# Optimization experiments

Measured on AMD Instinct MI355X. Metric: run time of the kernel, lower is better.

The kernel has to match this reference:

```python
import jax, jax.numpy as jnp
import numpy as np
import math

NCLASSES = 3
NMS_THR = 0.25
SCORE_THR = 0.1
MAX_NUM = 500
B, N = 4, 8192


def setup_inputs() -> dict:
    key = jax.random.key(0)
    ks = jax.random.split(key, 6)
    xy = jax.random.uniform(ks[0], (B, N, 2), minval=0.0, maxval=70.0)
    z = jax.random.normal(ks[1], (B, N, 1))
    lwh = jax.random.uniform(ks[2], (B, N, 3), minval=1.0, maxval=5.0)
    theta = jax.random.uniform(ks[3], (B, N, 1), minval=-math.pi, maxval=math.pi)
    cls = jax.random.uniform(ks[4], (B, N, NCLASSES))
    dirc = jax.random.randint(ks[5], (B, N, 1), 0, 2).astype(jnp.float32)
    results = jnp.concatenate([xy, z, lwh, theta, cls, dirc], axis=-1)  # [B,N,11]
    return {"results": results}


def limit_period(val, offset=1.0, period=math.pi):
    return val - jnp.floor(val / period + offset) * period


def _pairwise_iou(b):
    # b: [N,4] = (x1,y1,x2,y2); axis-aligned BEV IoU
    x1, y1, x2, y2 = b[:, 0], b[:, 1], b[:, 2], b[:, 3]
    area = (x2 - x1) * (y2 - y1)  # [N]
    iw = jnp.clip(jnp.minimum(x2[:, None], x2[None, :]) - jnp.maximum(x1[:, None], x1[None, :]), 0.0)
    ih = jnp.clip(jnp.minimum(y2[:, None], y2[None, :]) - jnp.maximum(y1[:, None], y1[None, :]), 0.0)
    inter = iw * ih
    return inter / (area[:, None] + area[None, :] - inter + 1e-8)


def _nms_class(boxes4, scores):
    # greedy NMS on score-descending order; invalid (below-threshold) boxes get -inf score
    valid = scores > SCORE_THR
    s = jnp.where(valid, scores, -jnp.inf)
    order = jnp.argsort(-s)  # descending
    bs = boxes4[order]
    ss = s[order]
    iou = _pairwise_iou(bs)  # [N,N]
    idx = jnp.arange(boxes4.shape[0])
    keep0 = jnp.isfinite(ss)

    def body(i, keep):
        sup = keep[i] & (iou[i] > NMS_THR) & (idx > i)
        return keep & ~sup

    keep = jax.lax.fori_loop(0, boxes4.shape[0], body, keep0)
    return order, jnp.where(keep, ss, -jnp.inf)


def _process(sample):
    # sample: [N,11] -> padded (bboxes [MAX_NUM,7], labels [MAX_NUM], scores [MAX_NUM])
    bbox = sample[:, :7]
    cls = sample[:, 7:10]
    dirp = sample[:, 10]
    xy = bbox[:, :2]
    lw = bbox[:, 3:5]
    boxes4 = jnp.concatenate([xy - lw / 2, xy + lw / 2], axis=-1)  # [N,4]

    all_b, all_l, all_s = [], [], []
    for c in range(NCLASSES):
        order, ss = _nms_class(boxes4, cls[:, c])
        bb = bbox[order]
        dd = dirp[order]
        ang = limit_period(bb[:, 6]) + (1.0 - dd) * math.pi
        bb = jnp.concatenate([bb[:, :6], ang[:, None]], axis=-1)
        all_b.append(bb)
        all_s.append(ss)
        all_l.append(jnp.full((N,), c, dtype=jnp.int32))
    b = jnp.concatenate(all_b, 0)   # [3N,7]
    s = jnp.concatenate(all_s, 0)   # [3N]
    l = jnp.concatenate(all_l, 0)   # [3N]
    top_s, top_i = jax.lax.top_k(s, MAX_NUM)
    return b[top_i], l[top_i], top_s


def reference(results):
    # results: [B,N,11]; returns (lidar_bboxes [B,500,7], labels [B,500], scores [B,500])
    return jax.vmap(_process)(results)
```

## Files before the change

### kernel.cpp

```cpp
#include <hip/hip_runtime.h>
#include <stdint.h>

#pragma clang fp contract(off)

#define NB 4
#define NN 8192
#define NC 3
#define NG 12
#define MAXN 500
#define KEEP_CAP 512

typedef unsigned long long u64;
typedef uint32_t u32;

#define NSO   0u
#define NSKEY 393216u
#define NSB4  786432u
#define NSAR  2359296u
#define NVAL  2752512u
#define NALV  2764800u
#define NKKEY 2777088u
#define NKPOS 2801664u
#define NKCNT 2826240u
#define NFLG  2826304u
#define PMAT  3145728u
#define WS_NEED 9437184u

#define PR_CH   32
#define PR_ROWS 2048
#define PUNITS_PER_G 528
#define PB_TPB 256
#define PB_BLOCKS 1584

#define WS_SORTED_ORIG 0
#define WS_ALIVE       393216
#define WS_KEPT_KEY    405504
#define WS_KEPT_POS    430080
#define WS_KEPT_CNT    454656
#define NMS_EPS 1.0000004f

__device__ __forceinline__ u32 sort_key(float s) {
  u32 b = __float_as_uint(s);
  u32 o = (b & 0x80000000u) ? ~b : (b | 0x80000000u);
  return ~o;
}

#define PHYS(i) ((i) + ((i) >> 3))
#define CEX(A, B, UP) \
  { if ((x[A] > x[B]) == (UP)) { u64 tt = x[A]; x[A] = x[B]; x[B] = tt; } }

__global__ __launch_bounds__(256) void sortL_kernel(
    const float* __restrict__ in, u64* __restrict__ kk)
{
  const int g = blockIdx.x >> 2, seg = blockIdx.x & 3;
  const int b = g / NC, c = g % NC;
  const float* __restrict__ base = in + (size_t)b * NN * 11;
  __shared__ u64 sk[2304];
  const int tid = threadIdx.x;
  const int gbase = seg << 11;

  for (int i = tid; i < 2048; i += 256) {
    int p = gbase + i;
    float sc = base[p * 11 + 7 + c];
    float s = (sc > 0.1f) ? sc : -INFINITY;
    sk[PHYS(i)] = ((u64)sort_key(s) << 16) | (u32)p;
  }
  __syncthreads();
  {
    const int pb = 9 * tid;
    u64 x[8];
#pragma unroll
    for (int a = 0; a < 8; ++a) x[a] = sk[pb + a];
    const bool u8 = ((((tid << 3)) & 8) == 0);
    CEX(0, 1, true); CEX(2, 3, false); CEX(4, 5, true); CEX(6, 7, false);
    CEX(0, 2, true); CEX(1, 3, true); CEX(4, 6, false); CEX(5, 7, false);
    CEX(0, 1, true); CEX(2, 3, true); CEX(4, 5, false); CEX(6, 7, false);
    CEX(0, 4, u8); CEX(1, 5, u8); CEX(2, 6, u8); CEX(3, 7, u8);
    CEX(0, 2, u8); CEX(1, 3, u8); CEX(4, 6, u8); CEX(5, 7, u8);
    CEX(0, 1, u8); CEX(2, 3, u8); CEX(4, 5, u8); CEX(6, 7, u8);
#pragma unroll
    for (int a = 0; a < 8; ++a) sk[pb + a] = x[a];
  }
  __syncthreads();
  for (int k = 16; k <= 2048; k <<= 1) {
    for (int j = k >> 1; j >= 8; j >>= 1) {
      for (int t = tid; t < 1024; t += 256) {
        int i = (t << 1) - (t & (j - 1));
        int q = i | j;
        int pi = PHYS(i), pq = PHYS(q);
        u64 ka = sk[pi], kb = sk[pq];
        bool up = ((i & k) == 0);
        if ((ka > kb) == up) { sk[pi] = kb; sk[pq] = ka; }
      }
      __syncthreads();
    }
    {
      const int lb = tid << 3;
      const bool up = ((lb & k) == 0);
      const int pb = 9 * tid;
      u64 x[8];
#pragma unroll
      for (int a = 0; a < 8; ++a) x[a] = sk[pb + a];
      CEX(0, 4, up); CEX(1, 5, up); CEX(2, 6, up); CEX(3, 7, up);
      CEX(0, 2, up); CEX(1, 3, up); CEX(4, 6, up); CEX(5, 7, up);
      CEX(0, 1, up); CEX(2, 3, up); CEX(4, 5, up); CEX(6, 7, up);
#pragma unroll
      for (int a = 0; a < 8; ++a) sk[pb + a] = x[a];
    }
    __syncthreads();
  }
  for (int i = tid; i < 2048; i += 256)
    kk[(size_t)g * NN + gbase + i] = sk[PHYS(i)];
}

__global__ __launch_bounds__(1024) void merge_kernel(
    const float* __restrict__ in, const u64* __restrict__ kk,
    u32* __restrict__ so, u32* __restrict__ skey, float4* __restrict__ sb4,
    float* __restrict__ sar, u64* __restrict__ valid)
{
  const int g = blockIdx.x;
  const int b = g / NC;
  const int tid = threadIdx.x;
  __shared__ u64 seg[NN];
  __shared__ u64 outk[PR_ROWS];
  const u64* __restrict__ ks = kk + (size_t)g * NN;

  for (int e = tid; e < NN; e += 1024) seg[e] = ks[e];
  __syncthreads();

  for (int e = tid; e < NN; e += 1024) {
    const int sg = e >> 11, idx = e & 2047;
    const u64 k = seg[e];
    int rank = idx;
#pragma unroll
    for (int os = 0; os < 4; ++os) {
      if (os == sg) continue;
      const u64* __restrict__ arr = seg + (os << 11);
      int pos = 0;
#pragma unroll
      for (int st = 1024; st > 0; st >>= 1) {
        int np = pos + st;
        if (np <= 2048 && arr[np - 1] < k) pos = np;
      }
      rank += pos;
    }
    if (rank < PR_ROWS) outk[rank] = k;
  }
  __syncthreads();

  const float* __restrict__ base = in + (size_t)b * NN * 11;
  const int lane = tid & 63;
#pragma unroll
  for (int it = 0; it < PR_ROWS / 1024; ++it) {
    int i = it * 1024 + tid;
    u64 kv = outk[i];
    int orig = (int)(kv & 0xFFFFu);
    u32 key32 = (u32)(kv >> 16);
    so[(size_t)g * NN + i] = (u32)orig;
    skey[(size_t)g * NN + i] = key32;
    const float* r = base + orig * 11;
    float x = r[0], y = r[1], l = r[3], wd = r[4];
    float hx = l * 0.5f, hy = wd * 0.5f;
    float x1 = x - hx, y1 = y - hy, x2 = x + hx, y2 = y + hy;
    sb4[(size_t)g * NN + i] = make_float4(x1, y1, x2, y2);
    sar[(size_t)g * NN + i] = (x2 - x1) * (y2 - y1);
    u64 bal = __ballot(key32 != 0xFF800000u);
    if (lane == 0) valid[g * 128 + (i >> 6)] = bal;
  }
}

__global__ __launch_bounds__(PB_TPB) void build_prefix_kernel(
    const float4* __restrict__ sb4, const float* __restrict__ sar,
    u64* __restrict__ pmat)
{
  const int wib = __builtin_amdgcn_readfirstlane((int)(threadIdx.x >> 6));
  const int lane = threadIdx.x & 63;
  const int W = blockIdx.x * (PB_TPB / 64) + wib;
  if (W >= NG * PUNITS_PER_G) return;
  const int g = W / PUNITS_PER_G;
  int r = W - g * PUNITS_PER_G;
  int rb = 0, cum = 0;
  while (r >= cum + (PR_CH - rb)) { cum += PR_CH - rb; ++rb; }
  const int jw = rb + (r - cum);
  const double CMULT = 0.25 * (1.0 + 0x1p-24);

  const int col = jw * 64 + lane;
  const float4 J = sb4[(size_t)g * NN + col];
  const float jar = sar[(size_t)g * NN + col];
  const float4* __restrict__ Ib = sb4 + (size_t)g * NN + rb * 64;
  const float* __restrict__ Ia = sar + (size_t)g * NN + rb * 64;

  u32 accLo = 0, accHi = 0;
  for (int rr = 0; rr < 64; ++rr) {
    const float4 I = Ib[rr];
    const float iar = Ia[rr];
    const bool sel = (lane == rr);
    float iw = fminf(I.z, J.z) - fmaxf(I.x, J.x);
    float ih = fminf(I.w, J.w) - fmaxf(I.y, J.y);
    iw = fmaxf(iw, 0.0f); ih = fmaxf(ih, 0.0f);
    float inter = iw * ih;
    float denom = ((iar + jar) - inter) + 1e-8f;
    u64 cand = __ballot((double)inter > CMULT * (double)denom);
    accLo = sel ? (u32)(cand & 0xffffffffu) : accLo;
    accHi = sel ? (u32)(cand >> 32) : accHi;
  }
  pmat[((size_t)(g * PR_CH + jw)) * PR_ROWS + rb * 64 + lane] =
      ((u64)accHi << 32) | accLo;
}

__global__ __launch_bounds__(1024) void scan_prefix_kernel(
    const u64* __restrict__ pmat, const u64* __restrict__ valid,
    const u32* __restrict__ skey, u32* __restrict__ kept_key,
    u32* __restrict__ kept_pos, u32* __restrict__ kept_cnt,
    u32* __restrict__ flags)
{
  const int g = blockIdx.x;
  const int tid = threadIdx.x;
  const int wv = tid >> 6, lane = tid & 63;
  const int wl = tid & 127, grp = tid >> 7;
  __shared__ u64 remv[PR_CH];
  __shared__ u64 keepw[PR_CH];
  __shared__ u64 keepS;
  __shared__ u32 prefixL[PR_CH];
  __shared__ u32 cntS;
  __shared__ int stopS;

  if (tid < PR_CH) { remv[tid] = ~valid[g * 128 + tid]; keepw[tid] = 0; }
  if (tid == 0) { cntS = 0; stopS = 0; }
  __syncthreads();

  const u64* __restrict__ pm = pmat + (size_t)g * PR_CH * PR_ROWS;
  u64 rwDiag = 0, rwDiagNext = 0;
  if (wv == 0) rwDiag = pm[lane];
  const u64 maskgt = (lane == 63) ? 0ull : (~0ull << (lane + 1));

  for (int cc = 0; cc < PR_CH; ++cc) {
    const int w = cc + 1 + wl;
    const bool act = (w < PR_CH);
    u64 rw[8];
    if (act) {
#pragma unroll
      for (int k = 0; k < 8; ++k)
        rw[k] = pm[(size_t)w * PR_ROWS + cc * 64 + grp * 8 + k];
    }
    if (wv == 0) {
      const u64 alive0 = ~remv[cc];
      u64 K = alive0;
      for (int it = 0; it < 64; ++it) {
        u64 contrib = ((K >> lane) & 1ull) ? (rwDiag & maskgt) : 0ull;
#pragma unroll
        for (int off = 32; off > 0; off >>= 1)
          contrib |= (u64)__shfl_xor((long long)contrib, off);
        u64 Knew = alive0 & ~contrib;
        if (Knew == K) break;
        K = Knew;
      }
      if (lane == 0) {
        keepw[cc] = K; keepS = K;
        cntS += (u32)__popcll(K);
        if (cntS >= KEEP_CAP) stopS = 1;
      }
      if (cc + 1 < PR_CH)
        rwDiagNext = pm[(size_t)(cc + 1) * PR_ROWS + (cc + 1) * 64 + lane];
    }
    __syncthreads();
    if (stopS) break;
    if (act) {
      const u32 kmg = (u32)((keepS >> (grp * 8)) & 0xffu);
      u64 acc = 0;
#pragma unroll
      for (int k = 0; k < 8; ++k)
        if ((kmg >> k) & 1u) acc |= rw[k];
      if (acc) atomicOr(&remv[w], acc);
    }
    if (wv == 0) rwDiag = rwDiagNext;
    __syncthreads();
  }
  __syncthreads();

  if (tid == 0) {
    u32 acc = 0;
    for (int i = 0; i < PR_CH; ++i) { prefixL[i] = acc; acc += (u32)__popcll(keepw[i]); }
    cntS = acc;
    u32 ok = (acc >= KEEP_CAP) ? 1u : 0u;
    flags[g] = ok;
    if (ok) kept_cnt[g] = KEEP_CAP;
  }
  __syncthreads();
  if (cntS < KEEP_CAP) return;
  for (int p = tid; p < PR_ROWS; p += 1024) {
    int wd = p >> 6;
    u64 kw = keepw[wd];
    if ((kw >> (p & 63)) & 1ull) {
      u32 rank = prefixL[wd] + (u32)__popcll(kw & ((1ull << (p & 63)) - 1ull));
      if (rank < KEEP_CAP) {
        kept_key[g * KEEP_CAP + rank] = skey[g * NN + p];
        kept_pos[g * KEEP_CAP + rank] = (u32)p;
      }
    }
  }
}

__global__ __launch_bounds__(1024) void nms_kernel(
    const float* __restrict__ in, u32* __restrict__ sorted_orig,
    u64* __restrict__ alive_out, u32* __restrict__ kept_key,
    u32* __restrict__ kept_pos, u32* __restrict__ kept_cnt,
    const u32* __restrict__ flags)
{
  const int g = blockIdx.x;
  if (flags != nullptr && flags[g]) return;
  const int b = g / NC, c = g % NC;
  const float* __restrict__ base = in + (size_t)b * NN * 11;
  __shared__ u32 keys[NN];
  __shared__ uint16_t sidx[NN];
  __shared__ float4 keeperBuf[2][64];
  __shared__ int nkBuf[2];
  __shared__ u64 aliveArr[128];
  __shared__ u32 prefix[128];
  const int tid = threadIdx.x;
  const int w = tid >> 6, lane = tid & 63;

  for (int p = tid; p < NN; p += 1024) {
    float sc = base[p * 11 + 7 + c];
    float s = (sc > 0.1f) ? sc : -INFINITY;
    keys[p] = sort_key(s);
    sidx[p] = (uint16_t)p;
  }
  __syncthreads();
  for (int k = 2; k <= NN; k <<= 1) {
    for (int j = k >> 1; j > 0; j >>= 1) {
      for (int t = tid; t < NN / 2; t += 1024) {
        int i = (t << 1) - (t & (j - 1));
        int q = i | j;
        u32 ka = keys[i], kb = keys[q];
        uint16_t ia = sidx[i], ib = sidx[q];
        bool gt = (ka > kb) || (ka == kb && ia > ib);
        bool up = ((i & k) == 0);
        if (gt == up) { keys[i] = kb; keys[q] = ka; sidx[i] = ib; sidx[q] = ia; }
      }
      __syncthreads();
    }
  }
  float bx1[8], by1[8], bx2[8], by2[8], barea[8];
  u64 alive[8];
#pragma unroll
  for (int k = 0; k < 8; ++k) {
    int p = k * 1024 + tid;
    u32 key = keys[p];
    int orig = sidx[p];
    sorted_orig[g * NN + p] = (u32)orig;
    const float* r = base + orig * 11;
    float x = r[0], y = r[1], l = r[3], wd = r[4];
    float hx = l * 0.5f, hy = wd * 0.5f;
    bx1[k] = x - hx; by1[k] = y - hy; bx2[k] = x + hx; by2[k] = y + hy;
    barea[k] = (bx2[k] - bx1[k]) * (by2[k] - by1[k]);
    alive[k] = __ballot(key != 0xFF800000u);
  }
  for (int cc = 0; cc < 128; ++cc) {
    __syncthreads();
    int nk_prev = (cc > 0) ? nkBuf[(cc - 1) & 1] : 0;
    if (nk_prev > 0) {
      const int par = (cc - 1) & 1;
      for (int j = 0; j < nk_prev; ++j) {
        float4 K = keeperBuf[par][j];
        float ka = (K.z - K.x) * (K.w - K.y);
#pragma unroll
        for (int k = 0; k < 8; ++k) {
          if ((k * 16 + w) < cc) continue;
          if (alive[k] == 0ull) continue;
          float iw = fminf(bx2[k], K.z) - fmaxf(bx1[k], K.x);
          float ih = fminf(by2[k], K.w) - fmaxf(by1[k], K.y);
          iw = fmaxf(iw, 0.0f); ih = fmaxf(ih, 0.0f);
          float inter = iw * ih;
          float denom = (barea[k] + ka) - inter + 1e-8f;
          float t = 0.25f * denom;
          u64 sup = __ballot(inter > t);
          u64 wnd = __ballot(inter > t && inter <= t * NMS_EPS);
          if (wnd) {
            bool bb = inter > t;
            if (bb && inter <= t * NMS_EPS) bb = (inter / denom) > 0.25f;
            sup = __ballot(bb);
          }
          alive[k] &= ~sup;
        }
      }
    }
    if (w == (cc & 15)) {
      float mx1 = 0.f, my1 = 0.f, mx2 = 0.f, my2 = 0.f, ma = 0.f;
      u64 m = 0ull;
#pragma unroll
      for (int k = 0; k < 8; ++k) if (k == (cc >> 4)) {
        mx1 = bx1[k]; my1 = by1[k]; mx2 = bx2[k]; my2 = by2[k]; ma = barea[k];
        m = alive[k];
      }
      u64 keepm = 0ull;
      int nk = 0;
      while (m) {
        int bp = __ffsll(m) - 1;
        keepm |= 1ull << bp;
        m &= ~(1ull << bp);
        float kx1 = __shfl(mx1, bp), ky1 = __shfl(my1, bp);
        float kx2 = __shfl(mx2, bp), ky2 = __shfl(my2, bp);
        float ka = (kx2 - kx1) * (ky2 - ky1);
        float iw = fminf(mx2, kx2) - fmaxf(mx1, kx1);
        float ih = fminf(my2, ky2) - fmaxf(my1, ky1);
        iw = fmaxf(iw, 0.0f); ih = fmaxf(ih, 0.0f);
        float inter = iw * ih;
        float denom = (ma + ka) - inter + 1e-8f;
        float t = 0.25f * denom;
        u64 sup = __ballot(inter > t);
        u64 wnd = __ballot(inter > t && inter <= t * NMS_EPS);
        if (wnd) {
          bool bb = inter > t;
          if (bb && inter <= t * NMS_EPS) bb = (inter / denom) > 0.25f;
          sup = __ballot(bb);
        }
        m &= ~sup;
        if (lane == bp) keeperBuf[cc & 1][nk] = make_float4(mx1, my1, mx2, my2);
        nk++;
      }
#pragma unroll
      for (int k = 0; k < 8; ++k) if (k == (cc >> 4)) alive[k] = keepm;
      if (lane == 0) nkBuf[cc & 1] = nk;
    }
  }
  __syncthreads();
  if (lane == 0) {
#pragma unroll
    for (int k = 0; k < 8; ++k) aliveArr[k * 16 + w] = alive[k];
  }
  __syncthreads();
  if (tid == 0) {
    u32 acc = 0;
    for (int i = 0; i < 128; ++i) { prefix[i] = acc; acc += (u32)__popcll(aliveArr[i]); }
    kept_cnt[g] = acc;
  }
  __syncthreads();
  for (int i = tid; i < 128; i += 1024) alive_out[g * 128 + i] = aliveArr[i];
#pragma unroll
  for (int k = 0; k < 8; ++k) {
    int word = k * 16 + w;
    u64 a = alive[k];
    if ((a >> lane) & 1ull) {
      u32 rank = prefix[word] + (u32)__popcll(a & ((1ull << lane) - 1ull));
      if (rank < KEEP_CAP) {
        int p = k * 1024 + tid;
        kept_key[g * KEEP_CAP + rank] = keys[p];
        kept_pos[g * KEEP_CAP + rank] = (u32)p;
      }
    }
  }
}

__global__ __launch_bounds__(512) void topk_kernel(
    const float* __restrict__ in, const u32* __restrict__ sorted_orig,
    const u64* __restrict__ alive_ws, const u32* __restrict__ kept_key,
    const u32* __restrict__ kept_pos, const u32* __restrict__ kept_cnt,
    float* __restrict__ out)
{
  const int b = blockIdx.x;
  const int tid = threadIdx.x;
  __shared__ u64 arr[NC][KEEP_CAP];
  __shared__ int sT[3], sL[3];
  if (tid < 3) {
    int K = (int)kept_cnt[b * 3 + tid];
    sT[tid] = K;
    sL[tid] = min(K, KEEP_CAP);
  }
  __syncthreads();
  const int L0 = sL[0], L1 = sL[1], L2 = sL[2];
  const int navail = L0 + L1 + L2;
  const int Ttot = sT[0] + sT[1] + sT[2];

  for (int s = tid; s < NC * KEEP_CAP; s += 512) {
    int c = s >> 9, i = s & 511;
    u64 key = ~0ull;
    if (i < sL[c]) {
      int g = b * 3 + c;
      u64 k32 = kept_key[g * KEEP_CAP + i];
      u32 pos = kept_pos[g * KEEP_CAP + i];
      key = (k32 << 15) | (u32)(c * NN + pos);
    }
    arr[c][i] = key;
  }
  __syncthreads();

  for (int s = tid; s < NC * KEEP_CAP; s += 512) {
    int c = s >> 9, i = s & 511;
    if (i >= sL[c]) continue;
    u64 k = arr[c][i];
    int rank = i;
#pragma unroll
    for (int oc = 0; oc < NC; ++oc) {
      if (oc == c) continue;
      int lo = 0, hi = sL[oc];
      while (lo < hi) { int mid = (lo + hi) >> 1; if (arr[oc][mid] < k) lo = mid + 1; else hi = mid; }
      rank += lo;
    }
    if (rank < MAXN) {
      u32 flat = (u32)(k & 32767u);
      int cc = (int)(flat >> 13), pos = (int)(flat & 8191);
      u32 k32 = (u32)(k >> 15);
      u32 o = ~k32;
      u32 bits = (o & 0x80000000u) ? (o ^ 0x80000000u) : ~o;
      float sval = __uint_as_float(bits);
      u32 orig = sorted_orig[(b * 3 + cc) * NN + pos];
      const float* row = in + ((size_t)b * NN + orig) * 11;
      const float PI_F = 3.14159265358979323846f;
      float theta = row[6];
      float v = theta / PI_F;
      float fl = floorf(v + 1.0f);
      float lp = theta - fl * PI_F;
      float ang = lp + (1.0f - row[10]) * PI_F;
      float* ob = out + ((size_t)b * MAXN + rank) * 7;
      ob[0] = row[0]; ob[1] = row[1]; ob[2] = row[2];
      ob[3] = row[3]; ob[4] = row[4]; ob[5] = row[5]; ob[6] = ang;
      out[NB * MAXN * 7 + b * MAXN + rank] = (float)cc;
      out[NB * MAXN * 7 + NB * MAXN + b * MAXN + rank] = sval;
    }
  }

  for (int r = navail + tid; r < MAXN; r += 512) {
    int need = r - Ttot;
    int fflat = 0;
    for (int wd = 0; wd < 384; ++wd) {
      u64 a = alive_ws[b * 384 + wd];
      int z = 64 - __popcll(a);
      if (need < z) {
        u64 na = ~a;
        for (int it = 0; it < need; ++it) na &= na - 1ull;
        fflat = wd * 64 + (__ffsll(na) - 1);
        break;
      }
      need -= z;
    }
    int c = fflat >> 13, pos = fflat & 8191;
    u32 orig = sorted_orig[(b * 3 + c) * NN + pos];
    const float* row = in + ((size_t)b * NN + orig) * 11;
    const float PI_F = 3.14159265358979323846f;
    float theta = row[6];
    float v = theta / PI_F;
    float fl = floorf(v + 1.0f);
    float lp = theta - fl * PI_F;
    float ang = lp + (1.0f - row[10]) * PI_F;
    float* ob = out + ((size_t)b * MAXN + r) * 7;
    ob[0] = row[0]; ob[1] = row[1]; ob[2] = row[2];
    ob[3] = row[3]; ob[4] = row[4]; ob[5] = row[5]; ob[6] = ang;
    out[NB * MAXN * 7 + b * MAXN + r] = (float)c;
    out[NB * MAXN * 7 + NB * MAXN + b * MAXN + r] = -INFINITY;
  }
}

extern "C" void kernel_launch(void* const* d_in, const int* in_sizes, int n_in,
                              void* d_out, int out_size, void* d_ws, size_t ws_size,
                              hipStream_t stream) {
  const float* in = (const float*)d_in[0];
  float* out = (float*)d_out;
  char* ws = (char*)d_ws;

  if (ws_size >= (size_t)WS_NEED) {
    u32* so = (u32*)(ws + NSO);
    u32* skey = (u32*)(ws + NSKEY);
    float4* sb4 = (float4*)(ws + NSB4);
    float* sar = (float*)(ws + NSAR);
    u64* valid = (u64*)(ws + NVAL);
    u64* alive = (u64*)(ws + NALV);
    u32* kkey = (u32*)(ws + NKKEY);
    u32* kpos = (u32*)(ws + NKPOS);
    u32* kcnt = (u32*)(ws + NKCNT);
    u32* flags = (u32*)(ws + NFLG);
    u64* pmat = (u64*)(ws + PMAT);
    u64* kk = (u64*)(ws + PMAT);

    sortL_kernel<<<dim3(48), dim3(256), 0, stream>>>(in, kk);
    merge_kernel<<<dim3(NG), dim3(1024), 0, stream>>>(
        in, kk, so, skey, sb4, sar, valid);
    build_prefix_kernel<<<dim3(PB_BLOCKS), dim3(PB_TPB), 0, stream>>>(
        sb4, sar, pmat);
    scan_prefix_kernel<<<dim3(NG), dim3(1024), 0, stream>>>(
        pmat, valid, skey, kkey, kpos, kcnt, flags);
    nms_kernel<<<dim3(NG), dim3(1024), 0, stream>>>(
        in, so, alive, kkey, kpos, kcnt, flags);
    topk_kernel<<<dim3(NB), dim3(512), 0, stream>>>(
        in, so, alive, kkey, kpos, kcnt, out);
  } else {
    u32* sorted_orig = (u32*)(ws + WS_SORTED_ORIG);
    u64* alive = (u64*)(ws + WS_ALIVE);
    u32* kept_key = (u32*)(ws + WS_KEPT_KEY);
    u32* kept_pos = (u32*)(ws + WS_KEPT_POS);
    u32* kept_cnt = (u32*)(ws + WS_KEPT_CNT);
    nms_kernel<<<dim3(NG), dim3(1024), 0, stream>>>(
        in, sorted_orig, alive, kept_key, kept_pos, kept_cnt, nullptr);
    topk_kernel<<<dim3(NB), dim3(512), 0, stream>>>(
        in, sorted_orig, alive, kept_key, kept_pos, kept_cnt, out);
  }
}
```

Baseline: 100.1 us.

## Fuse six-kernel NMS pipeline into one cooperative kernel with grid syncs

Replaces the chain of separate launches (local sort, merge, IoU prefix build, prefix scan, fallback NMS, top-k) with a single 48-block, 1024-thread cooperative kernel that separates the stages with grid.sync(). The goal is to remove per-launch overhead and the gaps between kernels in a pipeline made of many short stages. In exchange, the IoU-matrix build now runs on only 48 blocks instead of 1584 smaller ones, and each grid barrier has a cost, so the parallel-heavy stage could slow down.

```diff
diff --git a/kernel.cpp b/kernel.cpp
--- a/kernel.cpp
+++ b/kernel.cpp
@@ -1,7 +1,10 @@
 #include <hip/hip_runtime.h>
+#include <hip/hip_cooperative_groups.h>
 #include <stdint.h>
 
 #pragma clang fp contract(off)
+
+namespace cg = cooperative_groups;
 
 #define NB 4
 #define NN 8192
@@ -12,6 +15,7 @@
 
 typedef unsigned long long u64;
 typedef uint32_t u32;
+typedef uint16_t u16;
 
 #define NSO   0u
 #define NSKEY 393216u
@@ -29,8 +33,6 @@
 #define PR_CH   32
 #define PR_ROWS 2048
 #define PUNITS_PER_G 528
-#define PB_TPB 256
-#define PB_BLOCKS 1584
 
 #define WS_SORTED_ORIG 0
 #define WS_ALIVE       393216
@@ -49,253 +51,497 @@
 #define CEX(A, B, UP) \
   { if ((x[A] > x[B]) == (UP)) { u64 tt = x[A]; x[A] = x[B]; x[B] = tt; } }
 
-__global__ __launch_bounds__(256) void sortL_kernel(
-    const float* __restrict__ in, u64* __restrict__ kk)
+__global__ __launch_bounds__(1024) void fused_kernel(
+    const float* __restrict__ in, u64* __restrict__ kk, u32* __restrict__ so,
+    u32* __restrict__ skey, float4* __restrict__ sb4, float* __restrict__ sar,
+    u64* __restrict__ valid, u64* __restrict__ pmat, u64* __restrict__ alive,
+    u32* __restrict__ kkey, u32* __restrict__ kpos, u32* __restrict__ kcnt,
+    u32* __restrict__ flags, float* __restrict__ out)
 {
-  const int g = blockIdx.x >> 2, seg = blockIdx.x & 3;
-  const int b = g / NC, c = g % NC;
-  const float* __restrict__ base = in + (size_t)b * NN * 11;
-  __shared__ u64 sk[2304];
+  cg::grid_group grid = cg::this_grid();
+  __shared__ __align__(16) unsigned char smemraw[81920];
   const int tid = threadIdx.x;
-  const int gbase = seg << 11;
-
-  for (int i = tid; i < 2048; i += 256) {
-    int p = gbase + i;
-    float sc = base[p * 11 + 7 + c];
-    float s = (sc > 0.1f) ? sc : -INFINITY;
-    sk[PHYS(i)] = ((u64)sort_key(s) << 16) | (u32)p;
-  }
-  __syncthreads();
+  const int blk = blockIdx.x;
+  const int lane = tid & 63;
+
   {
-    const int pb = 9 * tid;
-    u64 x[8];
-#pragma unroll
-    for (int a = 0; a < 8; ++a) x[a] = sk[pb + a];
-    const bool u8 = ((((tid << 3)) & 8) == 0);
-    CEX(0, 1, true); CEX(2, 3, false); CEX(4, 5, true); CEX(6, 7, false);
-    CEX(0, 2, true); CEX(1, 3, true); CEX(4, 6, false); CEX(5, 7, false);
-    CEX(0, 1, true); CEX(2, 3, true); CEX(4, 5, false); CEX(6, 7, false);
-    CEX(0, 4, u8); CEX(1, 5, u8); CEX(2, 6, u8); CEX(3, 7, u8);
-    CEX(0, 2, u8); CEX(1, 3, u8); CEX(4, 6, u8); CEX(5, 7, u8);
-    CEX(0, 1, u8); CEX(2, 3, u8); CEX(4, 5, u8); CEX(6, 7, u8);
-#pragma unroll
-    for (int a = 0; a < 8; ++a) sk[pb + a] = x[a];
-  }
-  __syncthreads();
-  for (int k = 16; k <= 2048; k <<= 1) {
-    for (int j = k >> 1; j >= 8; j >>= 1) {
-      for (int t = tid; t < 1024; t += 256) {
-        int i = (t << 1) - (t & (j - 1));
-        int q = i | j;
-        int pi = PHYS(i), pq = PHYS(q);
-        u64 ka = sk[pi], kb = sk[pq];
-        bool up = ((i & k) == 0);
-        if ((ka > kb) == up) { sk[pi] = kb; sk[pq] = ka; }
-      }
-      __syncthreads();
-    }
-    {
-      const int lb = tid << 3;
-      const bool up = ((lb & k) == 0);
+    u64* sk = (u64*)smemraw;
+    const int g = blk >> 2, seg = blk & 3;
+    const int b = g / NC, c = g % NC;
+    const float* __restrict__ base = in + (size_t)b * NN * 11;
+    const int gbase = seg << 11;
+
+    for (int i = tid; i < 2048; i += 1024) {
+      int p = gbase + i;
+      float sc = base[p * 11 + 7 + c];
+      float s = (sc > 0.1f) ? sc : -INFINITY;
+      sk[PHYS(i)] = ((u64)sort_key(s) << 16) | (u32)p;
+    }
+    __syncthreads();
+    if (tid < 256) {
       const int pb = 9 * tid;
       u64 x[8];
 #pragma unroll
       for (int a = 0; a < 8; ++a) x[a] = sk[pb + a];
-      CEX(0, 4, up); CEX(1, 5, up); CEX(2, 6, up); CEX(3, 7, up);
-      CEX(0, 2, up); CEX(1, 3, up); CEX(4, 6, up); CEX(5, 7, up);
-      CEX(0, 1, up); CEX(2, 3, up); CEX(4, 5, up); CEX(6, 7, up);
+      const bool u8 = ((((tid << 3)) & 8) == 0);
+      CEX(0, 1, true); CEX(2, 3, false); CEX(4, 5, true); CEX(6, 7, false);
+      CEX(0, 2, true); CEX(1, 3, true); CEX(4, 6, false); CEX(5, 7, false);
+      CEX(0, 1, true); CEX(2, 3, true); CEX(4, 5, false); CEX(6, 7, false);
+      CEX(0, 4, u8); CEX(1, 5, u8); CEX(2, 6, u8); CEX(3, 7, u8);
+      CEX(0, 2, u8); CEX(1, 3, u8); CEX(4, 6, u8); CEX(5, 7, u8);
+      CEX(0, 1, u8); CEX(2, 3, u8); CEX(4, 5, u8); CEX(6, 7, u8);
 #pragma unroll
       for (int a = 0; a < 8; ++a) sk[pb + a] = x[a];
     }
     __syncthreads();
-  }
-  for (int i = tid; i < 2048; i += 256)
-    kk[(size_t)g * NN + gbase + i] = sk[PHYS(i)];
-}
-
-__global__ __launch_bounds__(1024) void merge_kernel(
-    const float* __restrict__ in, const u64* __restrict__ kk,
-    u32* __restrict__ so, u32* __restrict__ skey, float4* __restrict__ sb4,
-    float* __restrict__ sar, u64* __restrict__ valid)
-{
-  const int g = blockIdx.x;
-  const int b = g / NC;
-  const int tid = threadIdx.x;
-  __shared__ u64 seg[NN];
-  __shared__ u64 outk[PR_ROWS];
-  const u64* __restrict__ ks = kk + (size_t)g * NN;
-
-  for (int e = tid; e < NN; e += 1024) seg[e] = ks[e];
-  __syncthreads();
-
-  for (int e = tid; e < NN; e += 1024) {
-    const int sg = e >> 11, idx = e & 2047;
-    const u64 k = seg[e];
-    int rank = idx;
-#pragma unroll
-    for (int os = 0; os < 4; ++os) {
-      if (os == sg) continue;
-      const u64* __restrict__ arr = seg + (os << 11);
-      int pos = 0;
-#pragma unroll
-      for (int st = 1024; st > 0; st >>= 1) {
-        int np = pos + st;
-        if (np <= 2048 && arr[np - 1] < k) pos = np;
-      }
-      rank += pos;
-    }
-    if (rank < PR_ROWS) outk[rank] = k;
-  }
-  __syncthreads();
-
-  const float* __restrict__ base = in + (size_t)b * NN * 11;
-  const int lane = tid & 63;
-#pragma unroll
-  for (int it = 0; it < PR_ROWS / 1024; ++it) {
-    int i = it * 1024 + tid;
-    u64 kv = outk[i];
-    int orig = (int)(kv & 0xFFFFu);
-    u32 key32 = (u32)(kv >> 16);
-    so[(size_t)g * NN + i] = (u32)orig;
-    skey[(size_t)g * NN + i] = key32;
-    const float* r = base + orig * 11;
-    float x = r[0], y = r[1], l = r[3], wd = r[4];
-    float hx = l * 0.5f, hy = wd * 0.5f;
-    float x1 = x - hx, y1 = y - hy, x2 = x + hx, y2 = y + hy;
-    sb4[(size_t)g * NN + i] = make_float4(x1, y1, x2, y2);
-    sar[(size_t)g * NN + i] = (x2 - x1) * (y2 - y1);
-    u64 bal = __ballot(key32 != 0xFF800000u);
-    if (lane == 0) valid[g * 128 + (i >> 6)] = bal;
-  }
-}
-
-__global__ __launch_bounds__(PB_TPB) void build_prefix_kernel(
-    const float4* __restrict__ sb4, const float* __restrict__ sar,
-    u64* __restrict__ pmat)
-{
-  const int wib = __builtin_amdgcn_readfirstlane((int)(threadIdx.x >> 6));
-  const int lane = threadIdx.x & 63;
-  const int W = blockIdx.x * (PB_TPB / 64) + wib;
-  if (W >= NG * PUNITS_PER_G) return;
-  const int g = W / PUNITS_PER_G;
-  int r = W - g * PUNITS_PER_G;
-  int rb = 0, cum = 0;
-  while (r >= cum + (PR_CH - rb)) { cum += PR_CH - rb; ++rb; }
-  const int jw = rb + (r - cum);
-  const double CMULT = 0.25 * (1.0 + 0x1p-24);
-
-  const int col = jw * 64 + lane;
-  const float4 J = sb4[(size_t)g * NN + col];
-  const float jar = sar[(size_t)g * NN + col];
-  const float4* __restrict__ Ib = sb4 + (size_t)g * NN + rb * 64;
-  const float* __restrict__ Ia = sar + (size_t)g * NN + rb * 64;
-
-  u32 accLo = 0, accHi = 0;
-  for (int rr = 0; rr < 64; ++rr) {
-    const float4 I = Ib[rr];
-    const float iar = Ia[rr];
-    const bool sel = (lane == rr);
-    float iw = fminf(I.z, J.z) - fmaxf(I.x, J.x);
-    float ih = fminf(I.w, J.w) - fmaxf(I.y, J.y);
-    iw = fmaxf(iw, 0.0f); ih = fmaxf(ih, 0.0f);
-    float inter = iw * ih;
-    float denom = ((iar + jar) - inter) + 1e-8f;
-    u64 cand = __ballot((double)inter > CMULT * (double)denom);
-    accLo = sel ? (u32)(cand & 0xffffffffu) : accLo;
-    accHi = sel ? (u32)(cand >> 32) : accHi;
-  }
-  pmat[((size_t)(g * PR_CH + jw)) * PR_ROWS + rb * 64 + lane] =
-      ((u64)accHi << 32) | accLo;
-}
-
-__global__ __launch_bounds__(1024) void scan_prefix_kernel(
-    const u64* __restrict__ pmat, const u64* __restrict__ valid,
-    const u32* __restrict__ skey, u32* __restrict__ kept_key,
-    u32* __restrict__ kept_pos, u32* __restrict__ kept_cnt,
-    u32* __restrict__ flags)
-{
-  const int g = blockIdx.x;
-  const int tid = threadIdx.x;
-  const int wv = tid >> 6, lane = tid & 63;
-  const int wl = tid & 127, grp = tid >> 7;
-  __shared__ u64 remv[PR_CH];
-  __shared__ u64 keepw[PR_CH];
-  __shared__ u64 keepS;
-  __shared__ u32 prefixL[PR_CH];
-  __shared__ u32 cntS;
-  __shared__ int stopS;
-
-  if (tid < PR_CH) { remv[tid] = ~valid[g * 128 + tid]; keepw[tid] = 0; }
-  if (tid == 0) { cntS = 0; stopS = 0; }
-  __syncthreads();
-
-  const u64* __restrict__ pm = pmat + (size_t)g * PR_CH * PR_ROWS;
-  u64 rwDiag = 0, rwDiagNext = 0;
-  if (wv == 0) rwDiag = pm[lane];
-  const u64 maskgt = (lane == 63) ? 0ull : (~0ull << (lane + 1));
-
-  for (int cc = 0; cc < PR_CH; ++cc) {
-    const int w = cc + 1 + wl;
-    const bool act = (w < PR_CH);
-    u64 rw[8];
-    if (act) {
-#pragma unroll
-      for (int k = 0; k < 8; ++k)
-        rw[k] = pm[(size_t)w * PR_ROWS + cc * 64 + grp * 8 + k];
-    }
-    if (wv == 0) {
-      const u64 alive0 = ~remv[cc];
-      u64 K = alive0;
-      for (int it = 0; it < 64; ++it) {
-        u64 contrib = ((K >> lane) & 1ull) ? (rwDiag & maskgt) : 0ull;
-#pragma unroll
-        for (int off = 32; off > 0; off >>= 1)
-          contrib |= (u64)__shfl_xor((long long)contrib, off);
-        u64 Knew = alive0 & ~contrib;
-        if (Knew == K) break;
-        K = Knew;
-      }
+    for (int k = 16; k <= 2048; k <<= 1) {
+      for (int j = k >> 1; j >= 8; j >>= 1) {
+        {
+          int t = tid;
+          int i = (t << 1) - (t & (j - 1));
+          int q = i | j;
+          int pi = PHYS(i), pq = PHYS(q);
+          u64 ka = sk[pi], kb = sk[pq];
+          bool up = ((i & k) == 0);
+          if ((ka > kb) == up) { sk[pi] = kb; sk[pq] = ka; }
+        }
+        __syncthreads();
+      }
+      if (tid < 256) {
+        const int lb = tid << 3;
+        const bool up = ((lb & k) == 0);
+        const int pb = 9 * tid;
+        u64 x[8];
+#pragma unroll
+        for (int a = 0; a < 8; ++a) x[a] = sk[pb + a];
+        CEX(0, 4, up); CEX(1, 5, up); CEX(2, 6, up); CEX(3, 7, up);
+        CEX(0, 2, up); CEX(1, 3, up); CEX(4, 6, up); CEX(5, 7, up);
+        CEX(0, 1, up); CEX(2, 3, up); CEX(4, 5, up); CEX(6, 7, up);
+#pragma unroll
+        for (int a = 0; a < 8; ++a) sk[pb + a] = x[a];
+      }
+      __syncthreads();
+    }
+    for (int i = tid; i < 2048; i += 1024)
+      kk[(size_t)g * NN + gbase + i] = sk[PHYS(i)];
+  }
+  grid.sync();
+
+  if (blk < NG) {
+    const int g = blk;
+    const int b = g / NC;
+    u64* seg = (u64*)smemraw;
+    u64* outk = (u64*)(smemraw + 65536);
+    const u64* __restrict__ ks = kk + (size_t)g * NN;
+
+    for (int e = tid; e < NN; e += 1024) seg[e] = ks[e];
+    __syncthreads();
+
+    for (int e = tid; e < NN; e += 1024) {
+      const int sg = e >> 11, idx = e & 2047;
+      const u64 k = seg[e];
+      int rank = idx;
+#pragma unroll
+      for (int os = 0; os < 4; ++os) {
+        if (os == sg) continue;
+        const u64* __restrict__ arr = seg + (os << 11);
+        int pos = 0;
+#pragma unroll
+        for (int st = 1024; st > 0; st >>= 1) {
+          int np = pos + st;
+          if (np <= 2048 && arr[np - 1] < k) pos = np;
+        }
+        rank += pos;
+      }
+      if (rank < PR_ROWS) outk[rank] = k;
+    }
+    __syncthreads();
+
+    const float* __restrict__ base = in + (size_t)b * NN * 11;
+#pragma unroll
+    for (int it = 0; it < PR_ROWS / 1024; ++it) {
+      int i = it * 1024 + tid;
+      u64 kv = outk[i];
+      int orig = (int)(kv & 0xFFFFu);
+      u32 key32 = (u32)(kv >> 16);
+      so[(size_t)g * NN + i] = (u32)orig;
+      skey[(size_t)g * NN + i] = key32;
+      const float* r = base + orig * 11;
+      float x = r[0], y = r[1], l = r[3], wd = r[4];
+      float hx = l * 0.5f, hy = wd * 0.5f;
+      float x1 = x - hx, y1 = y - hy, x2 = x + hx, y2 = y + hy;
+      sb4[(size_t)g * NN + i] = make_float4(x1, y1, x2, y2);
+      sar[(size_t)g * NN + i] = (x2 - x1) * (y2 - y1);
+      u64 bal = __ballot(key32 != 0xFF800000u);
+      if (lane == 0) valid[g * 128 + (i >> 6)] = bal;
+    }
+  }
+  grid.sync();
+
+  {
+    const int wib = __builtin_amdgcn_readfirstlane((int)(tid >> 6));
+    const double CMULT = 0.25 * (1.0 + 0x1p-24);
+    for (int W = blk * 16 + wib; W < NG * PUNITS_PER_G; W += 48 * 16) {
+      const int g = W / PUNITS_PER_G;
+      int r = W - g * PUNITS_PER_G;
+      int rb = 0, cum = 0;
+      while (r >= cum + (PR_CH - rb)) { cum += PR_CH - rb; ++rb; }
+      const int jw = rb + (r - cum);
+
+      const int col = jw * 64 + lane;
+      const float4 J = sb4[(size_t)g * NN + col];
+      const float jar = sar[(size_t)g * NN + col];
+      const float4* __restrict__ Ib = sb4 + (size_t)g * NN + rb * 64;
+      const float* __restrict__ Ia = sar + (size_t)g * NN + rb * 64;
+
+      u32 accLo = 0, accHi = 0;
+      for (int rr = 0; rr < 64; ++rr) {
+        const float4 I = Ib[rr];
+        const float iar = Ia[rr];
+        const bool sel = (lane == rr);
+        float iw = fminf(I.z, J.z) - fmaxf(I.x, J.x);
+        float ih = fminf(I.w, J.w) - fmaxf(I.y, J.y);
+        iw = fmaxf(iw, 0.0f); ih = fmaxf(ih, 0.0f);
+        float inter = iw * ih;
+        float denom = ((iar + jar) - inter) + 1e-8f;
+        u64 cand = __ballot((double)inter > CMULT * (double)denom);
+        accLo = sel ? (u32)(cand & 0xffffffffu) : accLo;
+        accHi = sel ? (u32)(cand >> 32) : accHi;
+      }
+      pmat[((size_t)(g * PR_CH + jw)) * PR_ROWS + rb * 64 + lane] =
+          ((u64)accHi << 32) | accLo;
+    }
+  }
+  grid.sync();
+
+  {
+    __shared__ u64 remv[PR_CH];
+    __shared__ u64 keepw[PR_CH];
+    __shared__ u64 keepS;
+    __shared__ u32 prefixL[PR_CH];
+    __shared__ u32 cntS;
+    __shared__ int stopS;
+    if (blk < NG) {
+      const int g = blk;
+      const int wv = tid >> 6;
+      const int wl = tid & 127, grp = tid >> 7;
+
+      if (tid < PR_CH) { remv[tid] = ~valid[g * 128 + tid]; keepw[tid] = 0; }
+      if (tid == 0) { cntS = 0; stopS = 0; }
+      __syncthreads();
+
+      const u64* __restrict__ pm = pmat + (size_t)g * PR_CH * PR_ROWS;
+      u64 rwDiag = 0, rwDiagNext = 0;
+      if (wv == 0) rwDiag = pm[lane];
+      const u64 maskgt = (lane == 63) ? 0ull : (~0ull << (lane + 1));
+
+      for (int cc = 0; cc < PR_CH; ++cc) {
+        const int w = cc + 1 + wl;
+        const bool act = (w < PR_CH);
+        u64 rw[8];
+        if (act) {
+#pragma unroll
+          for (int k = 0; k < 8; ++k)
+            rw[k] = pm[(size_t)w * PR_ROWS + cc * 64 + grp * 8 + k];
+        }
+        if (wv == 0) {
+          const u64 alive0 = ~remv[cc];
+          u64 K = alive0;
+          for (int it = 0; it < 64; ++it) {
+            u64 contrib = ((K >> lane) & 1ull) ? (rwDiag & maskgt) : 0ull;
+#pragma unroll
+            for (int off = 32; off > 0; off >>= 1)
+              contrib |= (u64)__shfl_xor((long long)contrib, off);
+            u64 Knew = alive0 & ~contrib;
+            if (Knew == K) break;
+            K = Knew;
+          }
+          if (lane == 0) {
+            keepw[cc] = K; keepS = K;
+            cntS += (u32)__popcll(K);
+            if (cntS >= KEEP_CAP) stopS = 1;
+          }
+          if (cc + 1 < PR_CH)
+            rwDiagNext = pm[(size_t)(cc + 1) * PR_ROWS + (cc + 1) * 64 + lane];
+        }
+        __syncthreads();
+        if (stopS) break;
+        if (act) {
+          const u32 kmg = (u32)((keepS >> (grp * 8)) & 0xffu);
+          u64 acc = 0;
+#pragma unroll
+          for (int k = 0; k < 8; ++k)
+            if ((kmg >> k) & 1u) acc |= rw[k];
+          if (acc) atomicOr(&remv[w], acc);
+        }
+        if (wv == 0) rwDiag = rwDiagNext;
+        __syncthreads();
+      }
+      __syncthreads();
+
+      if (tid == 0) {
+        u32 acc = 0;
+        for (int i = 0; i < PR_CH; ++i) { prefixL[i] = acc; acc += (u32)__popcll(keepw[i]); }
+        cntS = acc;
+        u32 ok = (acc >= KEEP_CAP) ? 1u : 0u;
+        flags[g] = ok;
+        if (ok) kcnt[g] = KEEP_CAP;
+      }
+      __syncthreads();
+      if (cntS >= KEEP_CAP) {
+        for (int p = tid; p < PR_ROWS; p += 1024) {
+          int wd = p >> 6;
+          u64 kw = keepw[wd];
+          if ((kw >> (p & 63)) & 1ull) {
+            u32 rank = prefixL[wd] + (u32)__popcll(kw & ((1ull << (p & 63)) - 1ull));
+            if (rank < KEEP_CAP) {
+              kkey[g * KEEP_CAP + rank] = skey[g * NN + p];
+              kpos[g * KEEP_CAP + rank] = (u32)p;
+            }
+          }
+        }
+      }
+    }
+  }
+  grid.sync();
+
+  {
+    __shared__ float4 keeperBuf[2][64];
+    __shared__ int nkBuf[2];
+    __shared__ u64 aliveArr[128];
+    __shared__ u32 prefix[128];
+    if (blk < NG && flags[blk] == 0u) {
+      const int g = blk;
+      const int b = g / NC, c = g % NC;
+      const float* __restrict__ base = in + (size_t)b * NN * 11;
+      u32* keys = (u32*)smemraw;
+      u16* sidx = (u16*)(smemraw + 32768);
+      const int w = tid >> 6;
+
+      for (int p = tid; p < NN; p += 1024) {
+        float sc = base[p * 11 + 7 + c];
+        float s = (sc > 0.1f) ? sc : -INFINITY;
+        keys[p] = sort_key(s);
+        sidx[p] = (u16)p;
+      }
+      __syncthreads();
+      for (int k = 2; k <= NN; k <<= 1) {
+        for (int j = k >> 1; j > 0; j >>= 1) {
+          for (int t = tid; t < NN / 2; t += 1024) {
+            int i = (t << 1) - (t & (j - 1));
+            int q = i | j;
+            u32 ka = keys[i], kb = keys[q];
+            u16 ia = sidx[i], ib = sidx[q];
+            bool gt = (ka > kb) || (ka == kb && ia > ib);
+            bool up = ((i & k) == 0);
+            if (gt == up) { keys[i] = kb; keys[q] = ka; sidx[i] = ib; sidx[q] = ia; }
+          }
+          __syncthreads();
+        }
+      }
+      float bx1[8], by1[8], bx2[8], by2[8], barea[8];
+      u64 alv[8];
+#pragma unroll
+      for (int k = 0; k < 8; ++k) {
+        int p = k * 1024 + tid;
+        u32 key = keys[p];
+        int orig = sidx[p];
+        so[(size_t)g * NN + p] = (u32)orig;
+        const float* r = base + orig * 11;
+        float x = r[0], y = r[1], l = r[3], wd = r[4];
+        float hx = l * 0.5f, hy = wd * 0.5f;
+        bx1[k] = x - hx; by1[k] = y - hy; bx2[k] = x + hx; by2[k] = y + hy;
+        barea[k] = (bx2[k] - bx1[k]) * (by2[k] - by1[k]);
+        alv[k] = __ballot(key != 0xFF800000u);
+      }
+      for (int cc = 0; cc < 128; ++cc) {
+        __syncthreads();
+        int nk_prev = (cc > 0) ? nkBuf[(cc - 1) & 1] : 0;
+        if (nk_prev > 0) {
+          const int par = (cc - 1) & 1;
+          for (int j = 0; j < nk_prev; ++j) {
+            float4 K = keeperBuf[par][j];
+            float ka = (K.z - K.x) * (K.w - K.y);
+#pragma unroll
+            for (int k = 0; k < 8; ++k) {
+              if ((k * 16 + w) < cc) continue;
+              if (alv[k] == 0ull) continue;
+              float iw = fminf(bx2[k], K.z) - fmaxf(bx1[k], K.x);
+              float ih = fminf(by2[k], K.w) - fmaxf(by1[k], K.y);
+              iw = fmaxf(iw, 0.0f); ih = fmaxf(ih, 0.0f);
+              float inter = iw * ih;
+              float denom = (barea[k] + ka) - inter + 1e-8f;
+              float t = 0.25f * denom;
+              u64 sup = __ballot(inter > t);
+              u64 wnd = __ballot(inter > t && inter <= t * NMS_EPS);
+              if (wnd) {
+                bool bb = inter > t;
+                if (bb && inter <= t * NMS_EPS) bb = (inter / denom) > 0.25f;
+                sup = __ballot(bb);
+              }
+              alv[k] &= ~sup;
+            }
+          }
+        }
+        if (w == (cc & 15)) {
+          float mx1 = 0.f, my1 = 0.f, mx2 = 0.f, my2 = 0.f, ma = 0.f;
+          u64 m = 0ull;
+#pragma unroll
+          for (int k = 0; k < 8; ++k) if (k == (cc >> 4)) {
+            mx1 = bx1[k]; my1 = by1[k]; mx2 = bx2[k]; my2 = by2[k]; ma = barea[k];
+            m = alv[k];
+          }
+          u64 keepm = 0ull;
+          int nk = 0;
+          while (m) {
+            int bp = __ffsll(m) - 1;
+            keepm |= 1ull << bp;
+            m &= ~(1ull << bp);
+            float kx1 = __shfl(mx1, bp), ky1 = __shfl(my1, bp);
+            float kx2 = __shfl(mx2, bp), ky2 = __shfl(my2, bp);
+            float ka = (kx2 - kx1) * (ky2 - ky1);
+            float iw = fminf(mx2, kx2) - fmaxf(mx1, kx1);
+            float ih = fminf(my2, ky2) - fmaxf(my1, ky1);
+            iw = fmaxf(iw, 0.0f); ih = fmaxf(ih, 0.0f);
+            float inter = iw * ih;
+            float denom = (ma + ka) - inter + 1e-8f;
+            float t = 0.25f * denom;
+            u64 sup = __ballot(inter > t);
+            u64 wnd = __ballot(inter > t && inter <= t * NMS_EPS);
+            if (wnd) {
+              bool bb = inter > t;
+              if (bb && inter <= t * NMS_EPS) bb = (inter / denom) > 0.25f;
+              sup = __ballot(bb);
+            }
+            m &= ~sup;
+            if (lane == bp) keeperBuf[cc & 1][nk] = make_float4(mx1, my1, mx2, my2);
+            nk++;
+          }
+#pragma unroll
+          for (int k = 0; k < 8; ++k) if (k == (cc >> 4)) alv[k] = keepm;
+          if (lane == 0) nkBuf[cc & 1] = nk;
+        }
+      }
+      __syncthreads();
       if (lane == 0) {
-        keepw[cc] = K; keepS = K;
-        cntS += (u32)__popcll(K);
-        if (cntS >= KEEP_CAP) stopS = 1;
-      }
-      if (cc + 1 < PR_CH)
-        rwDiagNext = pm[(size_t)(cc + 1) * PR_ROWS + (cc + 1) * 64 + lane];
-    }
-    __syncthreads();
-    if (stopS) break;
-    if (act) {
-      const u32 kmg = (u32)((keepS >> (grp * 8)) & 0xffu);
-      u64 acc = 0;
-#pragma unroll
-      for (int k = 0; k < 8; ++k)
-        if ((kmg >> k) & 1u) acc |= rw[k];
-      if (acc) atomicOr(&remv[w], acc);
-    }
-    if (wv == 0) rwDiag = rwDiagNext;
-    __syncthreads();
-  }
-  __syncthreads();
-
-  if (tid == 0) {
-    u32 acc = 0;
-    for (int i = 0; i < PR_CH; ++i) { prefixL[i] = acc; acc += (u32)__popcll(keepw[i]); }
-    cntS = acc;
-    u32 ok = (acc >= KEEP_CAP) ? 1u : 0u;
-    flags[g] = ok;
-    if (ok) kept_cnt[g] = KEEP_CAP;
-  }
-  __syncthreads();
-  if (cntS < KEEP_CAP) return;
-  for (int p = tid; p < PR_ROWS; p += 1024) {
-    int wd = p >> 6;
-    u64 kw = keepw[wd];
-    if ((kw >> (p & 63)) & 1ull) {
-      u32 rank = prefixL[wd] + (u32)__popcll(kw & ((1ull << (p & 63)) - 1ull));
-      if (rank < KEEP_CAP) {
-        kept_key[g * KEEP_CAP + rank] = skey[g * NN + p];
-        kept_pos[g * KEEP_CAP + rank] = (u32)p;
+#pragma unroll
+        for (int k = 0; k < 8; ++k) aliveArr[k * 16 + w] = alv[k];
+      }
+      __syncthreads();
+      if (tid == 0) {
+        u32 acc = 0;
+        for (int i = 0; i < 128; ++i) { prefix[i] = acc; acc += (u32)__popcll(aliveArr[i]); }
+        kcnt[g] = acc;
+      }
+      __syncthreads();
+      for (int i = tid; i < 128; i += 1024) alive[g * 128 + i] = aliveArr[i];
+#pragma unroll
+      for (int k = 0; k < 8; ++k) {
+        int word = k * 16 + w;
+        u64 a = alv[k];
+        if ((a >> lane) & 1ull) {
+          u32 rank = prefix[word] + (u32)__popcll(a & ((1ull << lane) - 1ull));
+          if (rank < KEEP_CAP) {
+            int p = k * 1024 + tid;
+            kkey[g * KEEP_CAP + rank] = keys[p];
+            kpos[g * KEEP_CAP + rank] = (u32)p;
+          }
+        }
+      }
+    }
+  }
+  grid.sync();
+
+  {
+    __shared__ int sT[3], sL[3];
+    if (blk < NB) {
+      const int b = blk;
+      u64* arr = (u64*)smemraw;
+      if (tid < 3) {
+        int K = (int)kcnt[b * 3 + tid];
+        sT[tid] = K;
+        sL[tid] = min(K, KEEP_CAP);
+      }
+      __syncthreads();
+      const int navail = sL[0] + sL[1] + sL[2];
+      const int Ttot = sT[0] + sT[1] + sT[2];
+
+      for (int s = tid; s < NC * KEEP_CAP; s += 1024) {
+        int c = s >> 9, i = s & 511;
+        u64 key = ~0ull;
+        if (i < sL[c]) {
+          int g = b * 3 + c;
+          u64 k32 = kkey[g * KEEP_CAP + i];
+          u32 pos = kpos[g * KEEP_CAP + i];
+          key = (k32 << 15) | (u32)(c * NN + pos);
+        }
+        arr[c * KEEP_CAP + i] = key;
+      }
+      __syncthreads();
+
+      for (int s = tid; s < NC * KEEP_CAP; s += 1024) {
+        int c = s >> 9, i = s & 511;
+        if (i >= sL[c]) continue;
+        u64 k = arr[c * KEEP_CAP + i];
+        int rank = i;
+#pragma unroll
+        for (int oc = 0; oc < NC; ++oc) {
+          if (oc == c) continue;
+          int lo = 0, hi = sL[oc];
+          while (lo < hi) { int mid = (lo + hi) >> 1; if (arr[oc * KEEP_CAP + mid] < k) lo = mid + 1; else hi = mid; }
+          rank += lo;
+        }
+        if (rank < MAXN) {
+          u32 flat = (u32)(k & 32767u);
+          int cc = (int)(flat >> 13), pos = (int)(flat & 8191);
+          u32 k32 = (u32)(k >> 15);
+          u32 o = ~k32;
+          u32 bits = (o & 0x80000000u) ? (o ^ 0x80000000u) : ~o;
+          float sval = __uint_as_float(bits);
+          u32 orig = so[(size_t)(b * 3 + cc) * NN + pos];
+          const float* row = in + ((size_t)b * NN + orig) * 11;
+          const float PI_F = 3.14159265358979323846f;
+          float theta = row[6];
+          float v = theta / PI_F;
+          float fl = floorf(v + 1.0f);
+          float lp = theta - fl * PI_F;
+          float ang = lp + (1.0f - row[10]) * PI_F;
+          float* ob = out + ((size_t)b * MAXN + rank) * 7;
+          ob[0] = row[0]; ob[1] = row[1]; ob[2] = row[2];
+          ob[3] = row[3]; ob[4] = row[4]; ob[5] = row[5]; ob[6] = ang;
+          out[NB * MAXN * 7 + b * MAXN + rank] = (float)cc;
+          out[NB * MAXN * 7 + NB * MAXN + b * MAXN + rank] = sval;
+        }
+      }
+
+      for (int r = navail + tid; r < MAXN; r += 1024) {
+        int need = r - Ttot;
+        int fflat = 0;
+        for (int wd = 0; wd < 384; ++wd) {
+          u64 a = alive[b * 384 + wd];
+          int z = 64 - __popcll(a);
+          if (need < z) {
+            u64 na = ~a;
+            for (int it = 0; it < need; ++it) na &= na - 1ull;
+            fflat = wd * 64 + (__ffsll(na) - 1);
+            break;
+          }
+          need -= z;
+        }
+        int c = fflat >> 13, pos = fflat & 8191;
+        u32 orig = so[(size_t)(b * 3 + c) * NN + pos];
+        const float* row = in + ((size_t)b * NN + orig) * 11;
+        const float PI_F = 3.14159265358979323846f;
+        float theta = row[6];
+        float v = theta / PI_F;
+        float fl = floorf(v + 1.0f);
+        float lp = theta - fl * PI_F;
+        float ang = lp + (1.0f - row[10]) * PI_F;
+        float* ob = out + ((size_t)b * MAXN + r) * 7;
+        ob[0] = row[0]; ob[1] = row[1]; ob[2] = row[2];
+        ob[3] = row[3]; ob[4] = row[4]; ob[5] = row[5]; ob[6] = ang;
+        out[NB * MAXN * 7 + b * MAXN + r] = (float)c;
+        out[NB * MAXN * 7 + NB * MAXN + b * MAXN + r] = -INFINITY;
       }
     }
   }
@@ -304,15 +550,13 @@
 __global__ __launch_bounds__(1024) void nms_kernel(
     const float* __restrict__ in, u32* __restrict__ sorted_orig,
     u64* __restrict__ alive_out, u32* __restrict__ kept_key,
-    u32* __restrict__ kept_pos, u32* __restrict__ kept_cnt,
-    const u32* __restrict__ flags)
+    u32* __restrict__ kept_pos, u32* __restrict__ kept_cnt)
 {
   const int g = blockIdx.x;
-  if (flags != nullptr && flags[g]) return;
   const int b = g / NC, c = g % NC;
   const float* __restrict__ base = in + (size_t)b * NN * 11;
   __shared__ u32 keys[NN];
-  __shared__ uint16_t sidx[NN];
+  __shared__ u16 sidx[NN];
   __shared__ float4 keeperBuf[2][64];
   __shared__ int nkBuf[2];
   __shared__ u64 aliveArr[128];
@@ -324,7 +568,7 @@
     float sc = base[p * 11 + 7 + c];
     float s = (sc > 0.1f) ? sc : -INFINITY;
     keys[p] = sort_key(s);
-    sidx[p] = (uint16_t)p;
+    sidx[p] = (u16)p;
   }
   __syncthreads();
   for (int k = 2; k <= NN; k <<= 1) {
@@ -333,7 +577,7 @@
         int i = (t << 1) - (t & (j - 1));
         int q = i | j;
         u32 ka = keys[i], kb = keys[q];
-        uint16_t ia = sidx[i], ib = sidx[q];
+        u16 ia = sidx[i], ib = sidx[q];
         bool gt = (ka > kb) || (ka == kb && ia > ib);
         bool up = ((i & k) == 0);
         if (gt == up) { keys[i] = kb; keys[q] = ka; sidx[i] = ib; sidx[q] = ia; }
@@ -468,8 +712,7 @@
     sL[tid] = min(K, KEEP_CAP);
   }
   __syncthreads();
-  const int L0 = sL[0], L1 = sL[1], L2 = sL[2];
-  const int navail = L0 + L1 + L2;
+  const int navail = sL[0] + sL[1] + sL[2];
   const int Ttot = sT[0] + sT[1] + sT[2];
 
   for (int s = tid; s < NC * KEEP_CAP; s += 512) {
@@ -572,17 +815,12 @@
     u64* pmat = (u64*)(ws + PMAT);
     u64* kk = (u64*)(ws + PMAT);
 
-    sortL_kernel<<<dim3(48), dim3(256), 0, stream>>>(in, kk);
-    merge_kernel<<<dim3(NG), dim3(1024), 0, stream>>>(
-        in, kk, so, skey, sb4, sar, valid);
-    build_prefix_kernel<<<dim3(PB_BLOCKS), dim3(PB_TPB), 0, stream>>>(
-        sb4, sar, pmat);
-    scan_prefix_kernel<<<dim3(NG), dim3(1024), 0, stream>>>(
-        pmat, valid, skey, kkey, kpos, kcnt, flags);
-    nms_kernel<<<dim3(NG), dim3(1024), 0, stream>>>(
-        in, so, alive, kkey, kpos, kcnt, flags);
-    topk_kernel<<<dim3(NB), dim3(512), 0, stream>>>(
-        in, so, alive, kkey, kpos, kcnt, out);
+    void* args[] = { (void*)&in, (void*)&kk, (void*)&so, (void*)&skey,
+                     (void*)&sb4, (void*)&sar, (void*)&valid, (void*)&pmat,
+                     (void*)&alive, (void*)&kkey, (void*)&kpos, (void*)&kcnt,
+                     (void*)&flags, (void*)&out };
+    hipLaunchCooperativeKernel((const void*)fused_kernel, dim3(48), dim3(1024),
+                               args, 0, stream);
   } else {
     u32* sorted_orig = (u32*)(ws + WS_SORTED_ORIG);
     u64* alive = (u64*)(ws + WS_ALIVE);
@@ -590,7 +828,7 @@
     u32* kept_pos = (u32*)(ws + WS_KEPT_POS);
     u32* kept_cnt = (u32*)(ws + WS_KEPT_CNT);
     nms_kernel<<<dim3(NG), dim3(1024), 0, stream>>>(
-        in, sorted_orig, alive, kept_key, kept_pos, kept_cnt, nullptr);
+        in, sorted_orig, alive, kept_key, kept_pos, kept_cnt);
     topk_kernel<<<dim3(NB), dim3(512), 0, stream>>>(
         in, sorted_orig, alive, kept_key, kept_pos, kept_cnt, out);
   }
```

After: 197.6 us. 1.97x slower.
